# Kernel optimization log

Measured on AMD Instinct MI355X. Metric: run time of the kernel, lower is better.

The kernel has to match this reference:

```python
import jax, jax.numpy as jnp
import numpy as np

N_NODES = 100000
N_EDGES = 1600000
N_GRAPHS = 64
IN_F, HID, OUT_F = 10, 128, 101


def setup_inputs() -> dict:
    key = jax.random.key(0)
    ks = jax.random.split(key, 12)
    x = jax.random.normal(ks[0], (N_NODES, IN_F), dtype=jnp.float32)
    edge_index = jax.random.randint(ks[1], (2, N_EDGES), 0, N_NODES, dtype=jnp.int64)
    batch = jnp.sort(jax.random.randint(ks[2], (N_NODES,), 0, N_GRAPHS, dtype=jnp.int64))
    def lin(k, fi, fo):
        s = 1.0 / np.sqrt(fi)
        return jax.random.uniform(k, (fi, fo), minval=-s, maxval=s, dtype=jnp.float32)
    W1 = lin(ks[3], IN_F, HID); b1 = jnp.zeros((HID,), jnp.float32)
    W2 = lin(ks[4], HID, HID); b2 = jnp.zeros((HID,), jnp.float32)
    W3 = lin(ks[5], HID, HID); b3 = jnp.zeros((HID,), jnp.float32)
    Wl = lin(ks[6], HID, OUT_F)
    bl = jax.random.uniform(ks[7], (OUT_F,), minval=-1/np.sqrt(HID), maxval=1/np.sqrt(HID), dtype=jnp.float32)
    return {"x": x, "edge_index": edge_index, "batch": batch,
            "W1": W1, "b1": b1, "W2": W2, "b2": b2, "W3": W3, "b3": b3,
            "Wl": Wl, "bl": bl}


def _gcn_norm(edge_index, n_nodes):
    # Add self-loops and compute symmetric normalization (PyG gcn_norm).
    loop = jnp.arange(n_nodes, dtype=edge_index.dtype)
    src = jnp.concatenate([edge_index[0], loop])
    dst = jnp.concatenate([edge_index[1], loop])
    deg = jax.ops.segment_sum(jnp.ones_like(dst, dtype=jnp.float32), dst, num_segments=n_nodes)
    dis = jnp.where(deg > 0, jax.lax.rsqrt(deg), 0.0)
    w = dis[src] * dis[dst]  # [E + N]
    return src, dst, w


def _gcn_conv(x, W, b, src, dst, w, n_nodes):
    h = x @ W                      # transform first (matches GCNConv)
    msg = h[src] * w[:, None]      # gather + edge normalize
    out = jax.ops.segment_sum(msg, dst, num_segments=n_nodes)  # scatter-add
    return out + b


def reference(x, edge_index, batch, W1, b1, W2, b2, W3, b3, Wl, bl):
    n = x.shape[0]
    src, dst, w = _gcn_norm(edge_index, n)
    h = jax.nn.relu(_gcn_conv(x, W1, b1, src, dst, w, n))
    h = jax.nn.relu(_gcn_conv(h, W2, b2, src, dst, w, n))
    h = _gcn_conv(h, W3, b3, src, dst, w, n)
    # global mean pool per graph
    sums = jax.ops.segment_sum(h, batch, num_segments=N_GRAPHS)
    cnts = jax.ops.segment_sum(jnp.ones((n,), jnp.float32), batch, num_segments=N_GRAPHS)
    pooled = sums / jnp.maximum(cnts, 1.0)[:, None]
    # dropout is identity in eval mode
    return pooled @ Wl + bl
```

## Files before the change

kernel.cpp:

```cpp
#include <hip/hip_runtime.h>
#include <hip/hip_bf16.h>

#define HID 128
#define OUTF 101
#define INF 10
#define XPAD 16

#define BUCK_SHIFT 8
#define NBUCK_MAX 512
#define BCAP 4608
#define FS_EPT 18
#define BS_TPB 256
#define BS_EPT 32
#define BS_EPB (BS_TPB * BS_EPT)

typedef __hip_bfloat16 bf16;
typedef __attribute__((ext_vector_type(8))) short short8;
typedef __attribute__((ext_vector_type(4))) float f32x4;

__device__ __forceinline__ float bflo(unsigned u) { return __uint_as_float(u << 16); }
__device__ __forceinline__ float bfhi(unsigned u) { return __uint_as_float(u & 0xffff0000u); }
__device__ __forceinline__ unsigned pk2(float a, float b) {
    __hip_bfloat162 t;
    t.x = __float2bfloat16(a);
    t.y = __float2bfloat16(b);
    return *reinterpret_cast<unsigned*>(&t);
}


__device__ __forceinline__ void wsplit_body(const float* __restrict__ W, bf16* __restrict__ wfh,
                                            bf16* __restrict__ wfl, int t) {
    int j    = t & 7;
    int lane = (t >> 3) & 63;
    int nt   = (t >> 9) & 7;
    int kb   = t >> 12;
    int k  = kb * 32 + (lane >> 4) * 8 + j;
    int nn = nt * 16 + (lane & 15);
    float w = W[k * HID + nn];
    float hi = __bfloat162float(__float2bfloat16(w));
    wfh[t] = __float2bfloat16(hi);
    wfl[t] = __float2bfloat16(w - hi);
}

__global__ void prep_kernel(const float* __restrict__ W2, bf16* __restrict__ wf2h,
                            bf16* __restrict__ wf2l,
                            const float* __restrict__ W3, bf16* __restrict__ wf3h,
                            bf16* __restrict__ wf3l,
                            int* __restrict__ gcur, int nbuck,
                            float* __restrict__ sums, int sums_n,
                            float* __restrict__ xps_dummy,
                            unsigned* __restrict__ hs_dummy)
{
    int b = blockIdx.x;
    int tid = threadIdx.x;
    if (b < 64) { wsplit_body(W2, wf2h, wf2l, b * 256 + tid); return; }
    b -= 64;
    if (b < 64) { wsplit_body(W3, wf3h, wf3l, b * 256 + tid); return; }
    b -= 64;
    if (b == 0) {
        for (int k = tid; k < nbuck; k += 256) gcur[k] = k * BCAP;
        return;
    }
    b -= 1;
    if (b < 8) {
        int t = b * 256 + tid;
        if (t * 4 < sums_n) ((float4*)sums)[t] = make_float4(0.f, 0.f, 0.f, 0.f);
        return;
    }
    if (tid < XPAD) xps_dummy[tid] = 0.f;
    if (tid < 64) hs_dummy[tid] = 0u;
}


__global__ __launch_bounds__(BS_TPB) void bucket_scatter_kernel(
        const int* __restrict__ src, const int* __restrict__ dst, int E,
        int* __restrict__ gcur, int2* __restrict__ estage, int nbuck) {
    __shared__ int cnt[NBUCK_MAX];
    __shared__ int base[NBUCK_MAX];
    int tid = threadIdx.x;
    int e0 = blockIdx.x * BS_EPB + tid;
    int ds[BS_EPT], ss[BS_EPT];
#pragma unroll
    for (int t = 0; t < BS_EPT; ++t) {
        int e = e0 + t * BS_TPB;
        ds[t] = (e < E) ? dst[e] : -1;
        ss[t] = (e < E) ? src[e] : 0;
    }
    for (int b = tid; b < NBUCK_MAX; b += BS_TPB) cnt[b] = 0;
    __syncthreads();
#pragma unroll
    for (int t = 0; t < BS_EPT; ++t)
        if (ds[t] >= 0) atomicAdd(&cnt[ds[t] >> BUCK_SHIFT], 1);
    __syncthreads();
    for (int b = tid; b < nbuck; b += BS_TPB) {
        int c = cnt[b];
        base[b] = c ? atomicAdd(&gcur[b], c) : 0;
    }
    __syncthreads();
    for (int b = tid; b < NBUCK_MAX; b += BS_TPB) cnt[b] = 0;
    __syncthreads();
#pragma unroll
    for (int t = 0; t < BS_EPT; ++t)
        if (ds[t] >= 0) {
            int bk = ds[t] >> BUCK_SHIFT;
            int o = atomicAdd(&cnt[bk], 1);
            estage[base[bk] + o] = make_int2(ss[t], ds[t]);
        }
}

__global__ __launch_bounds__(NBUCK_MAX) void scanb_kernel(const int* __restrict__ gcur,
                                                          int* __restrict__ bbase,
                                                          int* __restrict__ rowp,
                                                          int nbuck, int N) {
    __shared__ int sh[NBUCK_MAX];
    int t = threadIdx.x;
    sh[t] = (t < nbuck) ? (gcur[t] - t * BCAP) : 0;
    __syncthreads();
    for (int off = 1; off < NBUCK_MAX; off <<= 1) {
        int v = (t >= off) ? sh[t - off] : 0;
        __syncthreads();
        sh[t] += v;
        __syncthreads();
    }
    if (t < nbuck) bbase[t] = (t == 0) ? 0 : sh[t - 1];
    if (t == 0) {
        bbase[nbuck] = sh[nbuck - 1];
        rowp[N] = sh[nbuck - 1];
    }
}

__global__ __launch_bounds__(BS_TPB) void fine_scatter_kernel(
        const int2* __restrict__ estage, const int* __restrict__ bbase,
        float* __restrict__ dis, int* __restrict__ rowp,
        int* __restrict__ csrs, const float* __restrict__ x,
        float* __restrict__ xps, int n) {
    __shared__ int hist[256];
    __shared__ int pfx[256];
    __shared__ int lcur[256];
    __shared__ float sdis[256];
    int b = blockIdx.x;
    int tid = threadIdx.x;
    int node_lo = b << BUCK_SHIFT;
    int bb = bbase[b];
    int cnt = bbase[b + 1] - bb;
    int slo = b * BCAP;
    int2 regs[FS_EPT];
#pragma unroll
    for (int t = 0; t < FS_EPT; ++t) {
        int k = tid + t * BS_TPB;
        regs[t] = (k < cnt) ? estage[slo + k] : make_int2(0, -1);
    }
    hist[tid] = 0;
    __syncthreads();
#pragma unroll
    for (int t = 0; t < FS_EPT; ++t)
        if (regs[t].y >= 0) atomicAdd(&hist[regs[t].y & 255], 1);
    __syncthreads();
    int deg = hist[tid];
    int node = node_lo + tid;
    float dv = rsqrtf((float)(deg + 1));
    sdis[tid] = dv;
    if (node < n) dis[node] = dv;
    pfx[tid] = deg;
    __syncthreads();
    for (int off = 1; off < 256; off <<= 1) {
        int v = (tid >= off) ? pfx[tid - off] : 0;
        __syncthreads();
        pfx[tid] += v;
        __syncthreads();
    }
    int excl = (tid == 0) ? 0 : pfx[tid - 1];
    if (node < n) rowp[node] = bb + excl;
    lcur[tid] = excl;
    __syncthreads();
#pragma unroll
    for (int t = 0; t < FS_EPT; ++t)
        if (regs[t].y >= 0) {
            int pos = bb + atomicAdd(&lcur[regs[t].y & 255], 1);
            csrs[pos] = regs[t].x;
        }
#pragma unroll
    for (int t = 0; t < 16; ++t) {
        int idx = tid + t * 256;
        int nd = node_lo + (idx >> 4);
        int f = idx & 15;
        if (nd < n)
            xps[(size_t)nd * XPAD + f] = (f < INF) ? x[(size_t)nd * INF + f] * sdis[idx >> 4] : 0.f;
    }
}

__global__ __launch_bounds__(256) void aggxform10_kernel(
        const float* __restrict__ xps, const int* __restrict__ rowp,
        const int* __restrict__ csrs, const float* __restrict__ dis,
        const float* __restrict__ W1, const float* __restrict__ b1,
        bf16* __restrict__ h, int n) {
    int i = blockIdx.x * 4 + (threadIdx.x >> 6);
    if (i >= n) return;
    int lane = threadIdx.x & 63;
    int slot = lane >> 2;
    int c = lane & 3;
    float dd = dis[i];

    float acc[4];
    if (slot == 0) {
        float4 v = *(const float4*)(xps + (size_t)i * XPAD + c * 4);
        acc[0] = v.x; acc[1] = v.y; acc[2] = v.z; acc[3] = v.w;
    } else {
        acc[0] = acc[1] = acc[2] = acc[3] = 0.f;
    }

    int beg = rowp[i];
    int end = rowp[i + 1];
    for (int base = beg; base < end; base += 32) {
        int e0 = base + slot;
        int e1 = base + 16 + slot;
        int i0 = (e0 < end) ? e0 : end - 1;
        int i1 = (e1 < end) ? e1 : end - 1;
        int s0 = csrs[i0];
        int s1 = csrs[i1];
        s0 = (e0 < end) ? s0 : n;
        s1 = (e1 < end) ? s1 : n;
        float4 v0 = *(const float4*)(xps + (size_t)s0 * XPAD + c * 4);
        float4 v1 = *(const float4*)(xps + (size_t)s1 * XPAD + c * 4);
        acc[0] += v0.x + v1.x;
        acc[1] += v0.y + v1.y;
        acc[2] += v0.z + v1.z;
        acc[3] += v0.w + v1.w;
    }
#pragma unroll
    for (int j = 0; j < 4; ++j) {
        acc[j] += __shfl_xor(acc[j], 4, 64);
        acc[j] += __shfl_xor(acc[j], 8, 64);
        acc[j] += __shfl_xor(acc[j], 16, 64);
        acc[j] += __shfl_xor(acc[j], 32, 64);
        acc[j] *= dd;
    }

    float axk[INF];
#pragma unroll
    for (int k = 0; k < INF; ++k) axk[k] = __shfl(acc[k & 3], k >> 2, 4);

    int j0 = 2 * lane;
    float2 bb = *(const float2*)(b1 + j0);
    float r0 = bb.x, r1 = bb.y;
#pragma unroll
    for (int k = 0; k < INF; ++k) {
        float2 wv = *(const float2*)(W1 + k * HID + j0);
        r0 = fmaf(axk[k], wv.x, r0);
        r1 = fmaf(axk[k], wv.y, r1);
    }
    r0 = fmaxf(r0, 0.f);
    r1 = fmaxf(r1, 0.f);
    ((unsigned*)(h + (size_t)i * HID))[lane] = pk2(r0, r1);
}


__global__ __launch_bounds__(256) void lin128_mfma_kernel(
        const bf16* __restrict__ in, const bf16* __restrict__ wfh,
        const bf16* __restrict__ wfl, const float* __restrict__ dis,
        bf16* __restrict__ out, int n) {
    __shared__ short8 wh[2048];
    __shared__ short8 wl[2048];
    for (int v = threadIdx.x; v < 2048; v += 256) {
        wh[v] = ((const short8*)wfh)[v];
        wl[v] = ((const short8*)wfl)[v];
    }
    __syncthreads();

    int lane = threadIdx.x & 63;
    int wave = threadIdx.x >> 6;
    int col = lane & 15;
    int quad = lane >> 4;
    int m0 = blockIdx.x * 128 + wave * 32;

    f32x4 acc[2][8];
#pragma unroll
    for (int mt = 0; mt < 2; ++mt)
#pragma unroll
        for (int nt = 0; nt < 8; ++nt) acc[mt][nt] = (f32x4){0.f, 0.f, 0.f, 0.f};

    long rmax = n - 1;
    long r0 = m0 + col;        if (r0 > rmax) r0 = rmax;
    long r1 = m0 + 16 + col;   if (r1 > rmax) r1 = rmax;

#pragma unroll
    for (int kb = 0; kb < 4; ++kb) {
        int kofs = kb * 32 + quad * 8;
        short8 a0 = *(const short8*)(in + r0 * HID + kofs);
        short8 a1 = *(const short8*)(in + r1 * HID + kofs);
        int bbase = kb * 512 + lane;
#pragma unroll
        for (int nt = 0; nt < 8; ++nt) {
            short8 bh = wh[bbase + nt * 64];
            short8 bl = wl[bbase + nt * 64];
            acc[0][nt] = __builtin_amdgcn_mfma_f32_16x16x32_bf16(a0, bh, acc[0][nt], 0, 0, 0);
            acc[1][nt] = __builtin_amdgcn_mfma_f32_16x16x32_bf16(a1, bh, acc[1][nt], 0, 0, 0);
            acc[0][nt] = __builtin_amdgcn_mfma_f32_16x16x32_bf16(a0, bl, acc[0][nt], 0, 0, 0);
            acc[1][nt] = __builtin_amdgcn_mfma_f32_16x16x32_bf16(a1, bl, acc[1][nt], 0, 0, 0);
        }
    }

#pragma unroll
    for (int mt = 0; mt < 2; ++mt) {
        int mb = m0 + mt * 16 + quad * 4;
#pragma unroll
        for (int r = 0; r < 4; ++r) {
            int m = mb + r;
            if (m < n) {
                float dm = dis[m];
                bf16* orow = out + (size_t)m * HID + col;
#pragma unroll
                for (int nt = 0; nt < 8; ++nt)
                    orow[nt * 16] = __float2bfloat16(acc[mt][nt][r] * dm);
            }
        }
    }
}

__global__ __launch_bounds__(256) void agg128_kernel(
        const bf16* __restrict__ hs, const int* __restrict__ rowp,
        const int* __restrict__ csrs, const float* __restrict__ dis,
        const float* __restrict__ b, bf16* __restrict__ out, int n, int relu) {
    int i = blockIdx.x * 4 + (threadIdx.x >> 6);
    if (i >= n) return;
    int lane = threadIdx.x & 63;
    int slot = lane >> 4;
    int f = lane & 15;
    float dd = dis[i];

    float acc[8];
    if (slot == 0) {
        uint4 v = *(const uint4*)(hs + (size_t)i * HID + f * 8);
        acc[0] = bflo(v.x); acc[1] = bfhi(v.x);
        acc[2] = bflo(v.y); acc[3] = bfhi(v.y);
        acc[4] = bflo(v.z); acc[5] = bfhi(v.z);
        acc[6] = bflo(v.w); acc[7] = bfhi(v.w);
    } else {
#pragma unroll
        for (int j = 0; j < 8; ++j) acc[j] = 0.f;
    }

    int beg = rowp[i];
    int end = rowp[i + 1];
    for (int base = beg; base < end; base += 16) {
        int s[4];
#pragma unroll
        for (int u = 0; u < 4; ++u) {
            int e = base + u * 4 + slot;
            int idx = (e < end) ? e : end - 1;
            int sv = csrs[idx];
            s[u] = (e < end) ? sv : n;
        }
        uint4 v[4];
#pragma unroll
        for (int u = 0; u < 4; ++u) v[u] = *(const uint4*)(hs + (size_t)s[u] * HID + f * 8);
#pragma unroll
        for (int u = 0; u < 4; ++u) {
            acc[0] += bflo(v[u].x); acc[1] += bfhi(v[u].x);
            acc[2] += bflo(v[u].y); acc[3] += bfhi(v[u].y);
            acc[4] += bflo(v[u].z); acc[5] += bfhi(v[u].z);
            acc[6] += bflo(v[u].w); acc[7] += bfhi(v[u].w);
        }
    }

#pragma unroll
    for (int j = 0; j < 8; ++j) {
        acc[j] += __shfl_xor(acc[j], 16, 64);
        acc[j] += __shfl_xor(acc[j], 32, 64);
    }

    float4 b0 = *(const float4*)(b + f * 8);
    float4 b1 = *(const float4*)(b + f * 8 + 4);
    float r[8];
    r[0] = fmaf(acc[0], dd, b0.x); r[1] = fmaf(acc[1], dd, b0.y);
    r[2] = fmaf(acc[2], dd, b0.z); r[3] = fmaf(acc[3], dd, b0.w);
    r[4] = fmaf(acc[4], dd, b1.x); r[5] = fmaf(acc[5], dd, b1.y);
    r[6] = fmaf(acc[6], dd, b1.z); r[7] = fmaf(acc[7], dd, b1.w);
    if (relu) {
#pragma unroll
        for (int j = 0; j < 8; ++j) r[j] = fmaxf(r[j], 0.f);
    }
    if (slot == 0) {
        uint4 pk;
        pk.x = pk2(r[0], r[1]);
        pk.y = pk2(r[2], r[3]);
        pk.z = pk2(r[4], r[5]);
        pk.w = pk2(r[6], r[7]);
        *(uint4*)(out + (size_t)i * HID + f * 8) = pk;
    }
}


__global__ void pool_kernel(const bf16* __restrict__ h, const int* __restrict__ batch, int n,
                            float* __restrict__ sums) {
    int g = blockIdx.x;
    int j = threadIdx.x;
    int lo = 0, hi = n;
    while (lo < hi) { int mid = (lo + hi) >> 1; if (batch[mid] < g) lo = mid + 1; else hi = mid; }
    int start = lo;
    lo = start; hi = n;
    while (lo < hi) { int mid = (lo + hi) >> 1; if (batch[mid] < g + 1) lo = mid + 1; else hi = mid; }
    int end = lo;
    float acc = 0.f;
    for (int i = start + blockIdx.y; i < end; i += gridDim.y)
        acc += __bfloat162float(h[(size_t)i * HID + j]);
    atomicAdd(&sums[g * HID + j], acc);
}

__global__ void final_kernel(const float* __restrict__ sums, const int* __restrict__ batch, int n,
                             const float* __restrict__ Wl, const float* __restrict__ bl,
                             float* __restrict__ out) {
    int g = blockIdx.x;
    int o = threadIdx.x;
    __shared__ float p[HID];
    int lo = 0, hi = n;
    while (lo < hi) { int mid = (lo + hi) >> 1; if (batch[mid] < g) lo = mid + 1; else hi = mid; }
    int start = lo;
    lo = start; hi = n;
    while (lo < hi) { int mid = (lo + hi) >> 1; if (batch[mid] < g + 1) lo = mid + 1; else hi = mid; }
    float cnt = fmaxf((float)(lo - start), 1.0f);
    p[o] = sums[g * HID + o] / cnt;
    __syncthreads();
    if (o < OUTF) {
        float acc = bl[o];
#pragma unroll 8
        for (int k = 0; k < HID; ++k) acc += p[k] * Wl[k * OUTF + o];
        out[g * OUTF + o] = acc;
    }
}


extern "C" void kernel_launch(void* const* d_in, const int* in_sizes, int n_in,
                              void* d_out, int out_size, void* d_ws, size_t ws_size,
                              hipStream_t stream) {
    const float* x   = (const float*)d_in[0];
    const int*   ei  = (const int*)d_in[1];
    const int*   bat = (const int*)d_in[2];
    const float* W1  = (const float*)d_in[3];
    const float* b1  = (const float*)d_in[4];
    const float* W2  = (const float*)d_in[5];
    const float* b2  = (const float*)d_in[6];
    const float* W3  = (const float*)d_in[7];
    const float* b3  = (const float*)d_in[8];
    const float* Wl  = (const float*)d_in[9];
    const float* bl  = (const float*)d_in[10];

    const int N = in_sizes[0] / INF;
    const int E = in_sizes[1] / 2;
    const int G = out_size / OUTF;
    const int* src = ei;
    const int* dst = ei + E;

    const int nbuck = (N + (1 << BUCK_SHIFT) - 1) >> BUCK_SHIFT;

    char* w = (char*)d_ws;
    bf16*  bufA   = (bf16*)w;  w += (size_t)(N + 1) * HID * 2;
    bf16*  bufB   = (bf16*)w;  w += (size_t)(N + 1) * HID * 2;
    float* dis    = (float*)w; w += (size_t)N * 4;
    int*   rowp   = (int*)w;   w += (size_t)(N + 8) * 4;
    int*   csrs   = (int*)w;   w += (size_t)E * 4;
    float* sums   = (float*)w; w += (size_t)G * HID * 4;
    int*   gcur   = (int*)w;   w += (size_t)(nbuck + 8) * 4;
    int*   bbase  = (int*)w;   w += (size_t)(nbuck + 8) * 4;
    bf16*  wf2h   = (bf16*)w;  w += (size_t)HID * HID * 2;
    bf16*  wf2l   = (bf16*)w;  w += (size_t)HID * HID * 2;
    bf16*  wf3h   = (bf16*)w;  w += (size_t)HID * HID * 2;
    bf16*  wf3l   = (bf16*)w;  w += (size_t)HID * HID * 2;
    int2*  estage = (int2*)bufA;
    float* xps    = (float*)bufB;

    const int sums_n = G * HID;
    prep_kernel<<<64 + 64 + 1 + 8 + 1, 256, 0, stream>>>(
        W2, wf2h, wf2l, W3, wf3h, wf3l, gcur, nbuck, sums, sums_n,
        xps + (size_t)N * XPAD, (unsigned*)(bufB + (size_t)N * HID));

    bucket_scatter_kernel<<<(E + BS_EPB - 1) / BS_EPB, BS_TPB, 0, stream>>>(src, dst, E, gcur,
                                                                            estage, nbuck);
    scanb_kernel<<<1, NBUCK_MAX, 0, stream>>>(gcur, bbase, rowp, nbuck, N);
    fine_scatter_kernel<<<nbuck, BS_TPB, 0, stream>>>(estage, bbase, dis, rowp, csrs, x, xps, N);

    aggxform10_kernel<<<(N + 3) / 4, 256, 0, stream>>>(xps, rowp, csrs, dis, W1, b1, bufA, N);
    lin128_mfma_kernel<<<(N + 127) / 128, 256, 0, stream>>>(bufA, wf2h, wf2l, dis, bufB, N);
    agg128_kernel<<<(N + 3) / 4, 256, 0, stream>>>(bufB, rowp, csrs, dis, b2, bufA, N, 1);
    lin128_mfma_kernel<<<(N + 127) / 128, 256, 0, stream>>>(bufA, wf3h, wf3l, dis, bufB, N);
    agg128_kernel<<<(N + 3) / 4, 256, 0, stream>>>(bufB, rowp, csrs, dis, b3, bufA, N, 0);

    pool_kernel<<<dim3(G, 32), HID, 0, stream>>>(bufA, bat, N, sums);
    final_kernel<<<G, HID, 0, stream>>>(sums, bat, N, Wl, bl, (float*)d_out);
}
```

Before: 356.5 us.

## Fuse final aggregation with mean pooling and pack staged edges into one int

The last GCN aggregation now accumulates each node's normalized result straight into per-graph pool sums, with a register partial flushed by atomics whenever the graph id changes. This removes the write and re-read of the final node feature buffer and one kernel launch; the bias b3 moves into final_kernel after the mean. The edge staging buffer also packs the source id (20 bits) and the local destination (8 bits) into a single int, halving staging traffic. The packing assumes node ids below 2^20, which holds for 100k nodes. Each wave now handles 8 nodes sequentially, which reduces parallelism in the last aggregation.

Result: slower. 462.8 us (+29.8%).

```diff
diff --git a/kernel.cpp b/kernel.cpp
--- a/kernel.cpp
+++ b/kernel.cpp
@@ -74,7 +74,7 @@
 
 __global__ __launch_bounds__(BS_TPB) void bucket_scatter_kernel(
         const int* __restrict__ src, const int* __restrict__ dst, int E,
-        int* __restrict__ gcur, int2* __restrict__ estage, int nbuck) {
+        int* __restrict__ gcur, int* __restrict__ estage, int nbuck) {
     __shared__ int cnt[NBUCK_MAX];
     __shared__ int base[NBUCK_MAX];
     int tid = threadIdx.x;
@@ -104,7 +104,7 @@
         if (ds[t] >= 0) {
             int bk = ds[t] >> BUCK_SHIFT;
             int o = atomicAdd(&cnt[bk], 1);
-            estage[base[bk] + o] = make_int2(ss[t], ds[t]);
+            estage[base[bk] + o] = ss[t] | ((ds[t] & 255) << 20);
         }
 }
 
@@ -130,7 +130,7 @@
 }
 
 __global__ __launch_bounds__(BS_TPB) void fine_scatter_kernel(
-        const int2* __restrict__ estage, const int* __restrict__ bbase,
+        const int* __restrict__ estage, const int* __restrict__ bbase,
         float* __restrict__ dis, int* __restrict__ rowp,
         int* __restrict__ csrs, const float* __restrict__ x,
         float* __restrict__ xps, int n) {
@@ -144,17 +144,17 @@
     int bb = bbase[b];
     int cnt = bbase[b + 1] - bb;
     int slo = b * BCAP;
-    int2 regs[FS_EPT];
+    int regs[FS_EPT];
 #pragma unroll
     for (int t = 0; t < FS_EPT; ++t) {
         int k = tid + t * BS_TPB;
-        regs[t] = (k < cnt) ? estage[slo + k] : make_int2(0, -1);
+        regs[t] = (k < cnt) ? estage[slo + k] : -1;
     }
     hist[tid] = 0;
     __syncthreads();
 #pragma unroll
     for (int t = 0; t < FS_EPT; ++t)
-        if (regs[t].y >= 0) atomicAdd(&hist[regs[t].y & 255], 1);
+        if (regs[t] >= 0) atomicAdd(&hist[(regs[t] >> 20) & 255], 1);
     __syncthreads();
     int deg = hist[tid];
     int node = node_lo + tid;
@@ -175,9 +175,9 @@
     __syncthreads();
 #pragma unroll
     for (int t = 0; t < FS_EPT; ++t)
-        if (regs[t].y >= 0) {
-            int pos = bb + atomicAdd(&lcur[regs[t].y & 255], 1);
-            csrs[pos] = regs[t].x;
+        if (regs[t] >= 0) {
+            int pos = bb + atomicAdd(&lcur[(regs[t] >> 20) & 255], 1);
+            csrs[pos] = regs[t] & 0xFFFFF;
         }
 #pragma unroll
     for (int t = 0; t < 16; ++t) {
@@ -254,7 +254,6 @@
     ((unsigned*)(h + (size_t)i * HID))[lane] = pk2(r0, r1);
 }
 
-
 __global__ __launch_bounds__(256) void lin128_mfma_kernel(
         const bf16* __restrict__ in, const bf16* __restrict__ wfh,
         const bf16* __restrict__ wfl, const float* __restrict__ dis,
@@ -390,24 +389,87 @@
     }
 }
 
-
-__global__ void pool_kernel(const bf16* __restrict__ h, const int* __restrict__ batch, int n,
-                            float* __restrict__ sums) {
-    int g = blockIdx.x;
-    int j = threadIdx.x;
-    int lo = 0, hi = n;
-    while (lo < hi) { int mid = (lo + hi) >> 1; if (batch[mid] < g) lo = mid + 1; else hi = mid; }
-    int start = lo;
-    lo = start; hi = n;
-    while (lo < hi) { int mid = (lo + hi) >> 1; if (batch[mid] < g + 1) lo = mid + 1; else hi = mid; }
-    int end = lo;
-    float acc = 0.f;
-    for (int i = start + blockIdx.y; i < end; i += gridDim.y)
-        acc += __bfloat162float(h[(size_t)i * HID + j]);
-    atomicAdd(&sums[g * HID + j], acc);
-}
+__global__ __launch_bounds__(256) void agg128_pool_kernel(
+        const bf16* __restrict__ hs, const int* __restrict__ rowp,
+        const int* __restrict__ csrs, const float* __restrict__ dis,
+        const int* __restrict__ batch, float* __restrict__ sums, int n) {
+    int lane = threadIdx.x & 63;
+    int wave = threadIdx.x >> 6;
+    int slot = lane >> 4;
+    int f = lane & 15;
+    int i0 = blockIdx.x * 32 + wave * 8;
+    if (i0 >= n) return;
+
+    float pool[8];
+#pragma unroll
+    for (int j = 0; j < 8; ++j) pool[j] = 0.f;
+    int g_cur = batch[i0];
+
+    for (int t = 0; t < 8; ++t) {
+        int i = i0 + t;
+        if (i >= n) break;
+        int g = batch[i];
+        if (g != g_cur) {
+            if (slot == 0) {
+#pragma unroll
+                for (int j = 0; j < 8; ++j)
+                    atomicAdd(&sums[g_cur * HID + f * 8 + j], pool[j]);
+            }
+#pragma unroll
+            for (int j = 0; j < 8; ++j) pool[j] = 0.f;
+            g_cur = g;
+        }
+        float dd = dis[i];
+        float acc[8];
+        if (slot == 0) {
+            uint4 v = *(const uint4*)(hs + (size_t)i * HID + f * 8);
+            acc[0] = bflo(v.x); acc[1] = bfhi(v.x);
+            acc[2] = bflo(v.y); acc[3] = bfhi(v.y);
+            acc[4] = bflo(v.z); acc[5] = bfhi(v.z);
+            acc[6] = bflo(v.w); acc[7] = bfhi(v.w);
+        } else {
+#pragma unroll
+            for (int j = 0; j < 8; ++j) acc[j] = 0.f;
+        }
+        int beg = rowp[i];
+        int end = rowp[i + 1];
+        for (int base = beg; base < end; base += 16) {
+            int s[4];
+#pragma unroll
+            for (int u = 0; u < 4; ++u) {
+                int e = base + u * 4 + slot;
+                int idx = (e < end) ? e : end - 1;
+                int sv = csrs[idx];
+                s[u] = (e < end) ? sv : n;
+            }
+            uint4 v[4];
+#pragma unroll
+            for (int u = 0; u < 4; ++u) v[u] = *(const uint4*)(hs + (size_t)s[u] * HID + f * 8);
+#pragma unroll
+            for (int u = 0; u < 4; ++u) {
+                acc[0] += bflo(v[u].x); acc[1] += bfhi(v[u].x);
+                acc[2] += bflo(v[u].y); acc[3] += bfhi(v[u].y);
+                acc[4] += bflo(v[u].z); acc[5] += bfhi(v[u].z);
+                acc[6] += bflo(v[u].w); acc[7] += bfhi(v[u].w);
+            }
+        }
+#pragma unroll
+        for (int j = 0; j < 8; ++j) {
+            acc[j] += __shfl_xor(acc[j], 16, 64);
+            acc[j] += __shfl_xor(acc[j], 32, 64);
+            pool[j] = fmaf(acc[j], dd, pool[j]);
+        }
+    }
+    if (slot == 0) {
+#pragma unroll
+        for (int j = 0; j < 8; ++j)
+            atomicAdd(&sums[g_cur * HID + f * 8 + j], pool[j]);
+    }
+}
+
 
 __global__ void final_kernel(const float* __restrict__ sums, const int* __restrict__ batch, int n,
+                             const float* __restrict__ b3,
                              const float* __restrict__ Wl, const float* __restrict__ bl,
                              float* __restrict__ out) {
     int g = blockIdx.x;
@@ -419,7 +481,7 @@
     lo = start; hi = n;
     while (lo < hi) { int mid = (lo + hi) >> 1; if (batch[mid] < g + 1) lo = mid + 1; else hi = mid; }
     float cnt = fmaxf((float)(lo - start), 1.0f);
-    p[o] = sums[g * HID + o] / cnt;
+    p[o] = sums[g * HID + o] / cnt + b3[o];
     __syncthreads();
     if (o < OUTF) {
         float acc = bl[o];
@@ -466,7 +528,7 @@
     bf16*  wf2l   = (bf16*)w;  w += (size_t)HID * HID * 2;
     bf16*  wf3h   = (bf16*)w;  w += (size_t)HID * HID * 2;
     bf16*  wf3l   = (bf16*)w;  w += (size_t)HID * HID * 2;
-    int2*  estage = (int2*)bufA;
+    int*   estage = (int*)bufA;
     float* xps    = (float*)bufB;
 
     const int sums_n = G * HID;
@@ -483,8 +545,7 @@
     lin128_mfma_kernel<<<(N + 127) / 128, 256, 0, stream>>>(bufA, wf2h, wf2l, dis, bufB, N);
     agg128_kernel<<<(N + 3) / 4, 256, 0, stream>>>(bufB, rowp, csrs, dis, b2, bufA, N, 1);
     lin128_mfma_kernel<<<(N + 127) / 128, 256, 0, stream>>>(bufA, wf3h, wf3l, dis, bufB, N);
-    agg128_kernel<<<(N + 3) / 4, 256, 0, stream>>>(bufB, rowp, csrs, dis, b3, bufA, N, 0);
-
-    pool_kernel<<<dim3(G, 32), HID, 0, stream>>>(bufA, bat, N, sums);
-    final_kernel<<<G, HID, 0, stream>>>(sums, bat, N, Wl, bl, (float*)d_out);
-}
+    agg128_pool_kernel<<<(N + 31) / 32, 256, 0, stream>>>(bufB, rowp, csrs, dis, bat, sums, N);
+
+    final_kernel<<<G, HID, 0, stream>>>(sums, bat, N, b3, Wl, bl, (float*)d_out);
+}
```
